# Kernel optimization log

Measured on AMD Instinct MI355X. Metric: run time of the kernel, lower is better.

The kernel has to match this reference:

```python
import jax, jax.numpy as jnp
import numpy as np

N_NODES = 100000
N_EDGES = 1000000
IN_DIM = 64
HID = 64
N_CLUSTER = 30
REG = 0.01


def glorot(key, shape):
    lim = np.sqrt(6.0 / (shape[0] + shape[1]))
    return jax.random.uniform(key, shape, jnp.float32, -lim, lim)


def setup_inputs() -> dict:
    key = jax.random.key(0)
    k1, k2, k3, k4, k5 = jax.random.split(key, 5)
    x = jax.random.normal(k1, (N_NODES, IN_DIM), jnp.float32)
    edge_index = jax.random.randint(k2, (2, N_EDGES), 0, N_NODES, jnp.int64)
    edge_attr = jax.random.uniform(k3, (N_EDGES,), jnp.float32)
    W1 = glorot(k4, (IN_DIM, HID))
    b1 = jnp.zeros((HID,), jnp.float32)
    W2 = glorot(k5, (HID, N_CLUSTER))
    b2 = jnp.zeros((N_CLUSTER,), jnp.float32)
    return {"x": x, "edge_index": edge_index, "edge_attr": edge_attr,
            "W1": W1, "b1": b1, "W2": W2, "b2": b2}


def gcn_conv(x, W, b, src, dst, w):
    # PyG GCNConv with edge weights: add self-loops (weight 1), symmetric norm.
    h = x @ W  # [N, out]
    deg = jax.ops.segment_sum(w, dst, num_segments=N_NODES) + 1.0  # self-loop
    dinv = jax.lax.rsqrt(deg)
    norm = dinv[src] * w * dinv[dst]  # [E]
    agg = jax.ops.segment_sum(norm[:, None] * h[src], dst, num_segments=N_NODES)
    agg = agg + h / deg[:, None]  # self-loop contribution: norm = 1/deg
    return agg + b


def reference(x, edge_index, edge_attr, W1, b1, W2, b2):
    src, dst = edge_index[0], edge_index[1]
    h = jax.nn.relu(gcn_conv(x, W1, b1, src, dst, edge_attr))
    # dropout p=0 -> identity
    X2 = gcn_conv(h, W2, b2, src, dst, edge_attr)
    FX = jax.nn.softmax(X2, axis=-1)  # [N, C]
    FF = jnp.sum(FX[src] * FX[dst], axis=-1)  # [E]
    NFX = jnp.log(1.0 - FX ** 2)  # [N, C]
    preg = -jnp.sum(jnp.log(1.0001 - jnp.exp(jnp.sum(NFX, axis=0))))
    loss = jnp.mean((FF - edge_attr) ** 2)
    return FX, loss + REG * preg
```

## Files before the change

kernel.cpp:

```cpp
#include <hip/hip_runtime.h>
#include <hip/hip_fp16.h>
#include <math.h>

#define N_NODES 100000
#define N_EDGES 1000000
#define IN_DIM 64
#define HID 64
#define NC 30
#define NCP 32
#define REG_C 0.01f

#define NTILES (N_NODES / 16)
#define NBUCK 391
#define EPB_A 2048
#define NBLK_A 489
#define GEMM_BLOCKS 512

typedef _Float16 half8 __attribute__((ext_vector_type(8)));
typedef _Float16 h16x4 __attribute__((ext_vector_type(4)));
typedef float f32x4 __attribute__((ext_vector_type(4)));
typedef float f32x2 __attribute__((ext_vector_type(2)));

__device__ __forceinline__ unsigned char enc_fp8(float v) {
    return (unsigned char)(__builtin_amdgcn_cvt_pk_fp8_f32(v, v, 0, false) & 0xFF);
}
__device__ __forceinline__ float dec_fp8(unsigned char b) {
    return __builtin_amdgcn_cvt_f32_fp8((int)b, 0);
}
__device__ __forceinline__ f32x4 dec_fp8x4(unsigned u) {
    f32x4 r;
    r[0] = __builtin_amdgcn_cvt_f32_fp8((int)u, 0);
    r[1] = __builtin_amdgcn_cvt_f32_fp8((int)u, 1);
    r[2] = __builtin_amdgcn_cvt_f32_fp8((int)u, 2);
    r[3] = __builtin_amdgcn_cvt_f32_fp8((int)u, 3);
    return r;
}
__device__ __forceinline__ float dot4_fp8(unsigned a, unsigned b) {
    float s = __builtin_amdgcn_cvt_f32_fp8((int)a, 0) * __builtin_amdgcn_cvt_f32_fp8((int)b, 0);
    s += __builtin_amdgcn_cvt_f32_fp8((int)a, 1) * __builtin_amdgcn_cvt_f32_fp8((int)b, 1);
    s += __builtin_amdgcn_cvt_f32_fp8((int)a, 2) * __builtin_amdgcn_cvt_f32_fp8((int)b, 2);
    s += __builtin_amdgcn_cvt_f32_fp8((int)a, 3) * __builtin_amdgcn_cvt_f32_fp8((int)b, 3);
    return s;
}

__global__ void hist_gemm(const int* __restrict__ dst, int* __restrict__ histT,
                          const float* __restrict__ X, const float* __restrict__ W,
                          unsigned char* __restrict__ H8) {
    if (blockIdx.x < NBLK_A) {
        __shared__ int cnt[NBUCK];
        for (int i = threadIdx.x; i < NBUCK; i += 256) cnt[i] = 0;
        __syncthreads();
        int e0 = blockIdx.x * EPB_A;
#pragma unroll
        for (int j = 0; j < 8; ++j) {
            int e = e0 + j * 256 + threadIdx.x;
            if (e < N_EDGES) atomicAdd(&cnt[dst[e] >> 8], 1);
        }
        __syncthreads();
        for (int b = threadIdx.x; b < NBUCK; b += 256)
            histT[b * NBLK_A + blockIdx.x] = cnt[b];
        return;
    }
    const int lane = threadIdx.x & 63;
    const int wave = threadIdx.x >> 6;
    const int qd = lane >> 4;
    const int l = lane & 15;
    half8 bfrag[2][4];
#pragma unroll
    for (int kb = 0; kb < 2; ++kb)
#pragma unroll
        for (int t = 0; t < 4; ++t)
#pragma unroll
            for (int j = 0; j < 8; ++j)
                bfrag[kb][t][j] = (_Float16)W[(kb * 32 + qd * 8 + j) * 64 + t * 16 + l];

    const int gb = blockIdx.x - NBLK_A;
    const int waveStride = GEMM_BLOCKS * 4;
    for (int ntile = gb * 4 + wave; ntile < NTILES; ntile += waveStride) {
        const int node0 = ntile * 16;
        const float* arow = X + (size_t)(node0 + l) * 64 + qd * 8;
        half8 af0, af1;
#pragma unroll
        for (int j = 0; j < 8; ++j) {
            af0[j] = (_Float16)arow[j];
            af1[j] = (_Float16)arow[32 + j];
        }
        f32x4 acc[4];
#pragma unroll
        for (int t = 0; t < 4; ++t) acc[t] = (f32x4){0.f, 0.f, 0.f, 0.f};
#pragma unroll
        for (int t = 0; t < 4; ++t) {
            acc[t] = __builtin_amdgcn_mfma_f32_16x16x32_f16(af0, bfrag[0][t], acc[t], 0, 0, 0);
            acc[t] = __builtin_amdgcn_mfma_f32_16x16x32_f16(af1, bfrag[1][t], acc[t], 0, 0, 0);
        }
#pragma unroll
        for (int t = 0; t < 4; ++t)
#pragma unroll
            for (int rr = 0; rr < 4; ++rr)
                H8[(size_t)(node0 + qd * 4 + rr) * 64 + t * 16 + l] = enc_fp8(acc[t][rr]);
    }
}

__global__ void scanA(int* __restrict__ histT, int* __restrict__ bucketTotal) {
    __shared__ int s[NBLK_A];
    int b = blockIdx.x;
    for (int i = threadIdx.x; i < NBLK_A; i += 256) s[i] = histT[b * NBLK_A + i];
    __syncthreads();
    if (threadIdx.x == 0) {
        int run = 0;
        for (int i = 0; i < NBLK_A; ++i) { int t = s[i]; s[i] = run; run += t; }
        bucketTotal[b] = run;
    }
    __syncthreads();
    for (int i = threadIdx.x; i < NBLK_A; i += 256) histT[b * NBLK_A + i] = s[i];
}

__global__ void scanB(const int* __restrict__ bucketTotal, int* __restrict__ bucketBase) {
    __shared__ int s[NBUCK];
    for (int i = threadIdx.x; i < NBUCK; i += 256) s[i] = bucketTotal[i];
    __syncthreads();
    if (threadIdx.x == 0) {
        int run = 0;
        for (int i = 0; i < NBUCK; ++i) { int t = s[i]; s[i] = run; run += t; }
    }
    __syncthreads();
    for (int i = threadIdx.x; i < NBUCK; i += 256) bucketBase[i] = s[i];
    if (threadIdx.x == 0) bucketBase[NBUCK] = N_EDGES;
}

__global__ void scatter_coarse(const int* __restrict__ src, const int* __restrict__ dst,
                               const float* __restrict__ w, const int* __restrict__ histT,
                               const int* __restrict__ bucketBase,
                               int2* __restrict__ sw, unsigned char* __restrict__ dl) {
    __shared__ int cur[NBUCK];
    int bl = blockIdx.x;
    for (int b = threadIdx.x; b < NBUCK; b += 256)
        cur[b] = bucketBase[b] + histT[b * NBLK_A + bl];
    __syncthreads();
    int e0 = bl * EPB_A;
#pragma unroll
    for (int j = 0; j < 8; ++j) {
        int e = e0 + j * 256 + threadIdx.x;
        if (e < N_EDGES) {
            int d = dst[e];
            int pos = atomicAdd(&cur[d >> 8], 1);
            sw[pos] = make_int2(src[e], __float_as_int(w[e]));
            dl[pos] = (unsigned char)(d & 255);
        }
    }
}

__global__ void bucket_deg(const int2* __restrict__ sw, const unsigned char* __restrict__ dl,
                           const int* __restrict__ bucketBase, float* __restrict__ dinv,
                           float* __restrict__ invdeg, int* __restrict__ rowptr) {
    __shared__ int cnt[256];
    __shared__ float degf[256];
    __shared__ int sc[256];
    int b = blockIdx.x, tid = threadIdx.x;
    cnt[tid] = 0; degf[tid] = 0.f;
    __syncthreads();
    int p0 = bucketBase[b], p1 = bucketBase[b + 1];
    for (int p = p0 + tid; p < p1; p += 256) {
        int d = dl[p];
        atomicAdd(&cnt[d], 1);
        atomicAdd(&degf[d], __int_as_float(sw[p].y));
    }
    __syncthreads();
    sc[tid] = cnt[tid];
    __syncthreads();
    for (int off = 1; off < 256; off <<= 1) {
        int t = (tid >= off) ? sc[tid - off] : 0;
        __syncthreads();
        sc[tid] += t;
        __syncthreads();
    }
    int node = b * 256 + tid;
    if (node < N_NODES) {
        float d = degf[tid] + 1.0f;
        dinv[node] = rsqrtf(d);
        invdeg[node] = 1.0f / d;
        rowptr[node] = p0 + sc[tid] - cnt[tid];
    }
    if (b == 0 && tid == 0) rowptr[N_NODES] = N_EDGES;
}

__global__ void bucket_scatter(const int2* __restrict__ sw, const unsigned char* __restrict__ dl,
                               const int* __restrict__ bucketBase, const int* __restrict__ rowptr,
                               const float* __restrict__ dinv,
                               int2* __restrict__ edata2, int2* __restrict__ wd) {
    __shared__ int cur[256];
    __shared__ float ldinv[256];
    int b = blockIdx.x, tid = threadIdx.x;
    int node = b * 256 + tid;
    if (node < N_NODES) { cur[tid] = rowptr[node]; ldinv[tid] = dinv[node]; }
    __syncthreads();
    int p0 = bucketBase[b], p1 = bucketBase[b + 1];
    for (int p = p0 + tid; p < p1; p += 256) {
        int d = dl[p];
        int2 r = sw[p];
        float wv = __int_as_float(r.y);
        float norm = dinv[r.x] * wv * ldinv[d];
        int pos = atomicAdd(&cur[d], 1);
        edata2[pos] = make_int2(r.x, __float_as_int(norm));
        wd[pos] = make_int2(r.y, b * 256 + d);
    }
}

__global__ void agg64_fused(const int* __restrict__ rowptr, const int2* __restrict__ edata2,
                            const unsigned char* __restrict__ H8, const float* __restrict__ invdeg,
                            const float* __restrict__ b1, _Float16* __restrict__ h2h) {
    int node = blockIdx.x * 4 + (threadIdx.x >> 6);
    if (node >= N_NODES) return;
    const int lane = threadIdx.x & 63;
    const int s = lane >> 4;
    const int q = lane & 15;
    int p = rowptr[node], end = rowptr[node + 1];
    float acc[4][4] = {};
    for (; p + 15 < end; p += 16) {
        int2 e[4];
#pragma unroll
        for (int g = 0; g < 4; ++g) e[g] = edata2[p + 4 * g + s];
        unsigned u[4];
#pragma unroll
        for (int g = 0; g < 4; ++g)
            u[g] = *(const unsigned*)(H8 + ((unsigned)e[g].x << 6) + (q << 2));
#pragma unroll
        for (int g = 0; g < 4; ++g) {
            float n = __int_as_float(e[g].y);
            f32x4 d = dec_fp8x4(u[g]);
#pragma unroll
            for (int j = 0; j < 4; ++j)
                acc[g][j] += n * d[j];
        }
    }
    {
        int r = end - p;
        int2 e[4];
#pragma unroll
        for (int g = 0; g < 4; ++g) {
            e[g] = make_int2(0, 0);
            if (4 * g + s < r) e[g] = edata2[p + 4 * g + s];
        }
        unsigned u[4];
#pragma unroll
        for (int g = 0; g < 4; ++g)
            u[g] = *(const unsigned*)(H8 + ((unsigned)e[g].x << 6) + (q << 2));
#pragma unroll
        for (int g = 0; g < 4; ++g) {
            float n = __int_as_float(e[g].y);
            f32x4 d = dec_fp8x4(u[g]);
#pragma unroll
            for (int j = 0; j < 4; ++j)
                acc[g][j] += n * d[j];
        }
    }
    float v[4];
#pragma unroll
    for (int j = 0; j < 4; ++j) {
        float t = (acc[0][j] + acc[1][j]) + (acc[2][j] + acc[3][j]);
        t += __shfl_xor(t, 16);
        t += __shfl_xor(t, 32);
        v[j] = t;
    }
    unsigned us = *(const unsigned*)(H8 + ((unsigned)node << 6) + (q << 2));
    float idg = invdeg[node];
    f32x4 bv = *(const f32x4*)(b1 + (q << 2));
    if (s == 0) {
        f32x4 ds = dec_fp8x4(us);
        h16x4 hv;
#pragma unroll
        for (int j = 0; j < 4; ++j) {
            float rj = v[j] + ds[j] * idg + bv[j];
            hv[j] = (_Float16)fmaxf(rj, 0.f);
        }
        *(h16x4*)(h2h + ((unsigned)node << 6) + (q << 2)) = hv;
    }
}

__global__ void linear30(const _Float16* __restrict__ H, const float* __restrict__ W2,
                         __half* __restrict__ HH16) {
    __shared__ float sW[64 * NC];
    __shared__ float sH[8 * 64];
    for (int i = threadIdx.x; i < 64 * NC; i += blockDim.x) sW[i] = W2[i];
    int node0 = blockIdx.x * 8;
    for (int i = threadIdx.x; i < 8 * 64; i += blockDim.x) {
        int n = node0 + (i >> 6);
        sH[i] = (n < N_NODES) ? (float)H[(size_t)n * 64 + (i & 63)] : 0.f;
    }
    __syncthreads();
    int ln = threadIdx.x >> 5;
    int c = threadIdx.x & 31;
    int node = node0 + ln;
    if (node < N_NODES) {
        float acc = 0.f;
        if (c < NC) {
#pragma unroll
            for (int k = 0; k < 64; ++k) acc += sH[ln * 64 + k] * sW[k * NC + c];
        }
        HH16[(size_t)node * NCP + c] = __float2half(acc);
    }
}

__global__ void agg30_softmax_colsum(const int* __restrict__ rowptr, const int2* __restrict__ edata2,
                                     const __half* __restrict__ HH16,
                                     const float* __restrict__ invdeg,
                                     const float* __restrict__ b2, float* __restrict__ FX,
                                     unsigned char* __restrict__ FX8,
                                     float* __restrict__ colsum_part) {
    const int lane = threadIdx.x & 63;
    const int waveInBlock = threadIdx.x >> 6;
    const int half = lane >> 5;
    const int c = lane & 31;
    const bool activeC = (c < NC);
    const int wavesTotal = gridDim.x * (blockDim.x >> 6);
    const int w0 = blockIdx.x * (blockDim.x >> 6) + waveInBlock;

    const float bb = activeC ? b2[c] : 0.f;
    float lacc = 0.f;

    for (int pair = w0; pair < N_NODES / 2; pair += wavesTotal) {
        const int node = pair * 2 + half;
        int p = rowptr[node], end = rowptr[node + 1];
        float acc[8];
#pragma unroll
        for (int k = 0; k < 8; ++k) acc[k] = 0.f;
        for (; p + 7 < end; p += 8) {
            int2 e[8];
#pragma unroll
            for (int k = 0; k < 8; ++k) e[k] = edata2[p + k];
#pragma unroll
            for (int k = 0; k < 8; ++k)
                acc[k] += __int_as_float(e[k].y) *
                          __half2float(HH16[(size_t)e[k].x * NCP + c]);
        }
        {
            int r = end - p;
            int2 e[8];
#pragma unroll
            for (int k = 0; k < 8; ++k) {
                e[k] = make_int2(0, 0);
                if (k < r) e[k] = edata2[p + k];
            }
#pragma unroll
            for (int k = 0; k < 8; ++k)
                acc[k] += __int_as_float(e[k].y) *
                          __half2float(HH16[(size_t)e[k].x * NCP + c]);
        }
        float accs = ((acc[0] + acc[1]) + (acc[2] + acc[3])) +
                     ((acc[4] + acc[5]) + (acc[6] + acc[7]));
        float selfv = __half2float(HH16[(size_t)node * NCP + c]);
        float x = activeC ? (accs + selfv * invdeg[node] + bb) : -INFINITY;
        float mx = x;
        for (int off = 16; off; off >>= 1) mx = fmaxf(mx, __shfl_xor(mx, off));
        float e = activeC ? expf(x - mx) : 0.f;
        float s = e;
        for (int off = 16; off; off >>= 1) s += __shfl_xor(s, off);
        float fx = e / s;
        if (activeC) {
            FX[(size_t)node * NC + c] = fx;
            FX8[(size_t)node * NCP + c] = enc_fp8(fx);
            lacc += log1pf(-fx * fx);
        } else {
            FX8[(size_t)node * NCP + c] = 0;
        }
    }
    lacc += __shfl_xor(lacc, 32);
    __shared__ float part[4][NC];
    if (half == 0 && activeC) part[waveInBlock][c] = lacc;
    __syncthreads();
    if (threadIdx.x < NC) {
        float v = part[0][threadIdx.x] + part[1][threadIdx.x] +
                  part[2][threadIdx.x] + part[3][threadIdx.x];
        atomicAdd(&colsum_part[(blockIdx.x & 63) * 32 + threadIdx.x], v);
    }
}

__global__ void edge_loss_sorted(const int2* __restrict__ edata2, const int2* __restrict__ wd,
                                 const unsigned char* __restrict__ FX8,
                                 float* __restrict__ mse_part) {
    int e = blockIdx.x * blockDim.x + threadIdx.x;
    float v = 0.f;
    if (e < N_EDGES) {
        int2 sn = edata2[e];
        int2 wdv = wd[e];
        const uint4* rs = (const uint4*)(FX8 + (size_t)sn.x * NCP);
        const uint4* rd = (const uint4*)(FX8 + (size_t)wdv.y * NCP);
        uint4 a0 = rs[0], a1 = rs[1];
        uint4 b0 = rd[0], b1 = rd[1];
        float ff = dot4_fp8(a0.x, b0.x) + dot4_fp8(a0.y, b0.y) +
                   dot4_fp8(a0.z, b0.z) + dot4_fp8(a0.w, b0.w) +
                   dot4_fp8(a1.x, b1.x) + dot4_fp8(a1.y, b1.y) +
                   dot4_fp8(a1.z, b1.z) + dot4_fp8(a1.w, b1.w);
        float diff = ff - __int_as_float(wdv.x);
        v = diff * diff;
    }
    for (int off = 32; off > 0; off >>= 1) v += __shfl_down(v, off);
    __shared__ float ps[4];
    int lane = threadIdx.x & 63, wv = threadIdx.x >> 6;
    if (lane == 0) ps[wv] = v;
    __syncthreads();
    if (threadIdx.x == 0)
        atomicAdd(&mse_part[blockIdx.x & 63], ps[0] + ps[1] + ps[2] + ps[3]);
}

__global__ void finalize(const float* __restrict__ colsum_part, const float* __restrict__ mse_part,
                         float* __restrict__ out_loss) {
    int t = threadIdx.x;
    float m = mse_part[t];
    for (int off = 32; off > 0; off >>= 1) m += __shfl_down(m, off);
    float term = 0.f;
    if (t < NC) {
        float s = 0.f;
        for (int k = 0; k < 64; ++k) s += colsum_part[k * 32 + t];
        term = logf(1.0001f - expf(s));
    }
    for (int off = 32; off > 0; off >>= 1) term += __shfl_down(term, off);
    if (t == 0)
        out_loss[0] = m / (float)N_EDGES - REG_C * term;
}

extern "C" void kernel_launch(void* const* d_in, const int* in_sizes, int n_in,
                              void* d_out, int out_size, void* d_ws, size_t ws_size,
                              hipStream_t stream) {
    const float* x  = (const float*)d_in[0];
    const int*   ei = (const int*)d_in[1];
    const float* ea = (const float*)d_in[2];
    const float* W1 = (const float*)d_in[3];
    const float* b1 = (const float*)d_in[4];
    const float* W2 = (const float*)d_in[5];
    const float* b2 = (const float*)d_in[6];
    const int* srcI = ei;
    const int* dstI = ei + N_EDGES;

    float* FX   = (float*)d_out;
    float* loss = FX + (size_t)N_NODES * NC;

    float* ws = (float*)d_ws;
    float*         dinv   = ws;
    float*         invdeg = ws + 100000;
    unsigned char* h8     = (unsigned char*)(ws + 200000);
    _Float16*      h2h    = (_Float16*)(ws + 1800000);
    __half*        hh16   = (__half*)(ws + 5000000);
    unsigned char* fx8    = (unsigned char*)(ws + 6600000);
    float*         colsum_part = ws + 7400000;
    float*         mse_part    = ws + 7402048;
    int*           rowptr = (int*)(ws + 7402112);
    int*           histT  = (int*)(ws + 7502114);
    int*           bucketTotal = (int*)(ws + 7693314);
    int*           bucketBase  = (int*)(ws + 7693706);
    int2*          sw     = (int2*)(ws + 7694098);
    unsigned char* dl     = (unsigned char*)(ws + 9694098);
    int2*          edata2 = (int2*)(ws + 9944098);
    int2*          wd     = (int2*)(ws + 11944098);

    hipMemsetAsync(colsum_part, 0, (2048 + 64) * sizeof(float), stream);

    hist_gemm<<<NBLK_A + GEMM_BLOCKS, 256, 0, stream>>>(dstI, histT, x, W1, h8);
    scanA<<<NBUCK, 256, 0, stream>>>(histT, bucketTotal);
    scanB<<<1, 256, 0, stream>>>(bucketTotal, bucketBase);
    scatter_coarse<<<NBLK_A, 256, 0, stream>>>(srcI, dstI, ea, histT, bucketBase, sw, dl);
    bucket_deg<<<NBUCK, 256, 0, stream>>>(sw, dl, bucketBase, dinv, invdeg, rowptr);
    bucket_scatter<<<NBUCK, 256, 0, stream>>>(sw, dl, bucketBase, rowptr, dinv, edata2, wd);
    agg64_fused<<<(N_NODES + 3) / 4, 256, 0, stream>>>(rowptr, edata2, h8, invdeg, b1, h2h);
    linear30<<<(N_NODES + 7) / 8, 256, 0, stream>>>(h2h, W2, hh16);
    agg30_softmax_colsum<<<4096, 256, 0, stream>>>(rowptr, edata2, hh16, invdeg, b2,
                                                   FX, fx8, colsum_part);
    edge_loss_sorted<<<(N_EDGES + 255) / 256, 256, 0, stream>>>(edata2, wd, fx8, mse_part);
    finalize<<<1, 64, 0, stream>>>(colsum_part, mse_part, loss);
}
```

Baseline: 295.4 us.

## Fuse W2 linear into layer-1 aggregation and drop sorted edge side array

Fuses the 64x30 linear projection into the layer-1 aggregation kernel using wave shuffles and shared W2, which removes the fp16 hidden buffer and a separate kernel launch. The second aggregation is remapped so each wave handles four nodes with two channels per lane, read as packed half2 loads. The edge loss now reads the original src/dst/weight arrays instead of a sorted wd array, so bucket_scatter no longer writes wd. The trade-off is that edge-loss gathers follow the original random edge order rather than dst-sorted order, and the fused kernel now loads all of W2 into shared memory in every block.

```diff
diff --git a/kernel.cpp b/kernel.cpp
--- a/kernel.cpp
+++ b/kernel.cpp
@@ -187,7 +187,7 @@
 __global__ void bucket_scatter(const int2* __restrict__ sw, const unsigned char* __restrict__ dl,
                                const int* __restrict__ bucketBase, const int* __restrict__ rowptr,
                                const float* __restrict__ dinv,
-                               int2* __restrict__ edata2, int2* __restrict__ wd) {
+                               int2* __restrict__ edata2) {
     __shared__ int cur[256];
     __shared__ float ldinv[256];
     int b = blockIdx.x, tid = threadIdx.x;
@@ -202,15 +202,18 @@
         float norm = dinv[r.x] * wv * ldinv[d];
         int pos = atomicAdd(&cur[d], 1);
         edata2[pos] = make_int2(r.x, __float_as_int(norm));
-        wd[pos] = make_int2(r.y, b * 256 + d);
     }
 }
 
 __global__ void agg64_fused(const int* __restrict__ rowptr, const int2* __restrict__ edata2,
                             const unsigned char* __restrict__ H8, const float* __restrict__ invdeg,
-                            const float* __restrict__ b1, _Float16* __restrict__ h2h) {
-    int node = blockIdx.x * 4 + (threadIdx.x >> 6);
-    if (node >= N_NODES) return;
+                            const float* __restrict__ b1, const float* __restrict__ W2,
+                            __half* __restrict__ HH16) {
+    __shared__ float sW[64 * NC + 2];
+    for (int i = threadIdx.x; i < 64 * NC; i += 256) sW[i] = W2[i];
+    if (threadIdx.x < 2) sW[64 * NC + threadIdx.x] = 0.f;
+
+    const int node = blockIdx.x * 4 + (threadIdx.x >> 6);
     const int lane = threadIdx.x & 63;
     const int s = lane >> 4;
     const int q = lane & 15;
@@ -265,40 +268,30 @@
     unsigned us = *(const unsigned*)(H8 + ((unsigned)node << 6) + (q << 2));
     float idg = invdeg[node];
     f32x4 bv = *(const f32x4*)(b1 + (q << 2));
-    if (s == 0) {
+    float hf[4];
+    {
         f32x4 ds = dec_fp8x4(us);
-        h16x4 hv;
 #pragma unroll
         for (int j = 0; j < 4; ++j) {
             float rj = v[j] + ds[j] * idg + bv[j];
-            hv[j] = (_Float16)fmaxf(rj, 0.f);
-        }
-        *(h16x4*)(h2h + ((unsigned)node << 6) + (q << 2)) = hv;
-    }
-}
-
-__global__ void linear30(const _Float16* __restrict__ H, const float* __restrict__ W2,
-                         __half* __restrict__ HH16) {
-    __shared__ float sW[64 * NC];
-    __shared__ float sH[8 * 64];
-    for (int i = threadIdx.x; i < 64 * NC; i += blockDim.x) sW[i] = W2[i];
-    int node0 = blockIdx.x * 8;
-    for (int i = threadIdx.x; i < 8 * 64; i += blockDim.x) {
-        int n = node0 + (i >> 6);
-        sH[i] = (n < N_NODES) ? (float)H[(size_t)n * 64 + (i & 63)] : 0.f;
-    }
-    __syncthreads();
-    int ln = threadIdx.x >> 5;
-    int c = threadIdx.x & 31;
-    int node = node0 + ln;
-    if (node < N_NODES) {
-        float acc = 0.f;
-        if (c < NC) {
-#pragma unroll
-            for (int k = 0; k < 64; ++k) acc += sH[ln * 64 + k] * sW[k * NC + c];
-        }
-        HH16[(size_t)node * NCP + c] = __float2half(acc);
-    }
+            hf[j] = (float)(_Float16)fmaxf(rj, 0.f);
+        }
+    }
+    __syncthreads();
+    const int ch = lane & 31;
+    float accw = 0.f;
+#pragma unroll
+    for (int qs = 0; qs < 8; ++qs) {
+        int q_src = ((lane >> 5) << 3) + qs;
+#pragma unroll
+        for (int j = 0; j < 4; ++j) {
+            float hk = __shfl(hf[j], q_src);
+            accw += hk * sW[(4 * q_src + j) * NC + ch];
+        }
+    }
+    accw += __shfl_xor(accw, 32);
+    if (lane < 32)
+        HH16[((size_t)node << 5) + ch] = (ch < NC) ? __float2half(accw) : __float2half(0.f);
 }
 
 __global__ void agg30_softmax_colsum(const int* __restrict__ rowptr, const int2* __restrict__ edata2,
@@ -309,64 +302,93 @@
                                      float* __restrict__ colsum_part) {
     const int lane = threadIdx.x & 63;
     const int waveInBlock = threadIdx.x >> 6;
-    const int half = lane >> 5;
-    const int c = lane & 31;
-    const bool activeC = (c < NC);
-    const int wavesTotal = gridDim.x * (blockDim.x >> 6);
-    const int w0 = blockIdx.x * (blockDim.x >> 6) + waveInBlock;
-
-    const float bb = activeC ? b2[c] : 0.f;
-    float lacc = 0.f;
-
-    for (int pair = w0; pair < N_NODES / 2; pair += wavesTotal) {
-        const int node = pair * 2 + half;
-        int p = rowptr[node], end = rowptr[node + 1];
-        float acc[8];
-#pragma unroll
-        for (int k = 0; k < 8; ++k) acc[k] = 0.f;
-        for (; p + 7 < end; p += 8) {
-            int2 e[8];
-#pragma unroll
-            for (int k = 0; k < 8; ++k) e[k] = edata2[p + k];
-#pragma unroll
-            for (int k = 0; k < 8; ++k)
-                acc[k] += __int_as_float(e[k].y) *
-                          __half2float(HH16[(size_t)e[k].x * NCP + c]);
-        }
-        {
-            int r = end - p;
-            int2 e[8];
-#pragma unroll
-            for (int k = 0; k < 8; ++k) {
-                e[k] = make_int2(0, 0);
-                if (k < r) e[k] = edata2[p + k];
-            }
-#pragma unroll
-            for (int k = 0; k < 8; ++k)
-                acc[k] += __int_as_float(e[k].y) *
-                          __half2float(HH16[(size_t)e[k].x * NCP + c]);
-        }
-        float accs = ((acc[0] + acc[1]) + (acc[2] + acc[3])) +
-                     ((acc[4] + acc[5]) + (acc[6] + acc[7]));
-        float selfv = __half2float(HH16[(size_t)node * NCP + c]);
-        float x = activeC ? (accs + selfv * invdeg[node] + bb) : -INFINITY;
-        float mx = x;
-        for (int off = 16; off; off >>= 1) mx = fmaxf(mx, __shfl_xor(mx, off));
-        float e = activeC ? expf(x - mx) : 0.f;
-        float s = e;
-        for (int off = 16; off; off >>= 1) s += __shfl_xor(s, off);
-        float fx = e / s;
-        if (activeC) {
-            FX[(size_t)node * NC + c] = fx;
-            FX8[(size_t)node * NCP + c] = enc_fp8(fx);
-            lacc += log1pf(-fx * fx);
-        } else {
-            FX8[(size_t)node * NCP + c] = 0;
-        }
-    }
-    lacc += __shfl_xor(lacc, 32);
-    __shared__ float part[4][NC];
-    if (half == 0 && activeC) part[waveInBlock][c] = lacc;
+    const int n = lane >> 4;
+    const int c2 = lane & 15;
+    const bool activeC = (c2 < 15);
+    const int node = (blockIdx.x * 4 + waveInBlock) * 4 + n;
+
+    float bb0 = activeC ? b2[2 * c2] : 0.f;
+    float bb1 = activeC ? b2[2 * c2 + 1] : 0.f;
+
+    int p = rowptr[node], end = rowptr[node + 1];
+    float a0[8], a1[8];
+#pragma unroll
+    for (int k = 0; k < 8; ++k) { a0[k] = 0.f; a1[k] = 0.f; }
+    const __half* __restrict__ Hc = HH16 + (c2 << 1);
+    for (; p + 7 < end; p += 8) {
+        int2 e[8];
+#pragma unroll
+        for (int k = 0; k < 8; ++k) e[k] = edata2[p + k];
+        unsigned h[8];
+#pragma unroll
+        for (int k = 0; k < 8; ++k)
+            h[k] = *(const unsigned*)(Hc + ((unsigned)e[k].x << 5));
+#pragma unroll
+        for (int k = 0; k < 8; ++k) {
+            float nw = __int_as_float(e[k].y);
+            float2 hf = __half22float2(*(const __half2*)&h[k]);
+            a0[k] += nw * hf.x;
+            a1[k] += nw * hf.y;
+        }
+    }
+    {
+        int r = end - p;
+        int2 e[8];
+#pragma unroll
+        for (int k = 0; k < 8; ++k) {
+            e[k] = make_int2(0, 0);
+            if (k < r) e[k] = edata2[p + k];
+        }
+        unsigned h[8];
+#pragma unroll
+        for (int k = 0; k < 8; ++k)
+            h[k] = *(const unsigned*)(Hc + ((unsigned)e[k].x << 5));
+#pragma unroll
+        for (int k = 0; k < 8; ++k) {
+            float nw = __int_as_float(e[k].y);
+            float2 hf = __half22float2(*(const __half2*)&h[k]);
+            a0[k] += nw * hf.x;
+            a1[k] += nw * hf.y;
+        }
+    }
+    float s0 = ((a0[0] + a0[1]) + (a0[2] + a0[3])) + ((a0[4] + a0[5]) + (a0[6] + a0[7]));
+    float s1 = ((a1[0] + a1[1]) + (a1[2] + a1[3])) + ((a1[4] + a1[5]) + (a1[6] + a1[7]));
+    unsigned hsu = *(const unsigned*)(Hc + ((unsigned)node << 5));
+    float2 hs = __half22float2(*(const __half2*)&hsu);
+    float idg = invdeg[node];
+    float x0 = activeC ? (s0 + hs.x * idg + bb0) : -INFINITY;
+    float x1 = activeC ? (s1 + hs.y * idg + bb1) : -INFINITY;
+    float mx = fmaxf(x0, x1);
+    mx = fmaxf(mx, __shfl_xor(mx, 1));
+    mx = fmaxf(mx, __shfl_xor(mx, 2));
+    mx = fmaxf(mx, __shfl_xor(mx, 4));
+    mx = fmaxf(mx, __shfl_xor(mx, 8));
+    float e0 = activeC ? expf(x0 - mx) : 0.f;
+    float e1 = activeC ? expf(x1 - mx) : 0.f;
+    float sum = e0 + e1;
+    sum += __shfl_xor(sum, 1);
+    sum += __shfl_xor(sum, 2);
+    sum += __shfl_xor(sum, 4);
+    sum += __shfl_xor(sum, 8);
+    float fx0 = e0 / sum;
+    float fx1 = e1 / sum;
+
+    if (activeC) {
+        *(f32x2*)(FX + (size_t)node * NC + 2 * c2) = (f32x2){fx0, fx1};
+        unsigned short pk = (unsigned short)((unsigned)enc_fp8(fx0) | ((unsigned)enc_fp8(fx1) << 8));
+        *(unsigned short*)(FX8 + ((unsigned)node << 5) + (c2 << 1)) = pk;
+    } else {
+        *(unsigned short*)(FX8 + ((unsigned)node << 5) + (c2 << 1)) = 0;
+    }
+    float lacc0 = activeC ? log1pf(-fx0 * fx0) : 0.f;
+    float lacc1 = activeC ? log1pf(-fx1 * fx1) : 0.f;
+    lacc0 += __shfl_xor(lacc0, 16); lacc0 += __shfl_xor(lacc0, 32);
+    lacc1 += __shfl_xor(lacc1, 16); lacc1 += __shfl_xor(lacc1, 32);
+    __shared__ float part[4][32];
+    if (lane < 16) {
+        part[waveInBlock][2 * c2] = lacc0;
+        part[waveInBlock][2 * c2 + 1] = lacc1;
+    }
     __syncthreads();
     if (threadIdx.x < NC) {
         float v = part[0][threadIdx.x] + part[1][threadIdx.x] +
@@ -375,23 +397,24 @@
     }
 }
 
-__global__ void edge_loss_sorted(const int2* __restrict__ edata2, const int2* __restrict__ wd,
-                                 const unsigned char* __restrict__ FX8,
-                                 float* __restrict__ mse_part) {
+__global__ void edge_loss_plain(const int* __restrict__ src, const int* __restrict__ dst,
+                                const float* __restrict__ w,
+                                const unsigned char* __restrict__ FX8,
+                                float* __restrict__ mse_part) {
     int e = blockIdx.x * blockDim.x + threadIdx.x;
     float v = 0.f;
     if (e < N_EDGES) {
-        int2 sn = edata2[e];
-        int2 wdv = wd[e];
-        const uint4* rs = (const uint4*)(FX8 + (size_t)sn.x * NCP);
-        const uint4* rd = (const uint4*)(FX8 + (size_t)wdv.y * NCP);
+        int sn = src[e];
+        int dn = dst[e];
+        const uint4* rs = (const uint4*)(FX8 + (size_t)sn * NCP);
+        const uint4* rd = (const uint4*)(FX8 + (size_t)dn * NCP);
         uint4 a0 = rs[0], a1 = rs[1];
         uint4 b0 = rd[0], b1 = rd[1];
         float ff = dot4_fp8(a0.x, b0.x) + dot4_fp8(a0.y, b0.y) +
                    dot4_fp8(a0.z, b0.z) + dot4_fp8(a0.w, b0.w) +
                    dot4_fp8(a1.x, b1.x) + dot4_fp8(a1.y, b1.y) +
                    dot4_fp8(a1.z, b1.z) + dot4_fp8(a1.w, b1.w);
-        float diff = ff - __int_as_float(wdv.x);
+        float diff = ff - w[e];
         v = diff * diff;
     }
     for (int off = 32; off > 0; off >>= 1) v += __shfl_down(v, off);
@@ -439,7 +462,6 @@
     float*         dinv   = ws;
     float*         invdeg = ws + 100000;
     unsigned char* h8     = (unsigned char*)(ws + 200000);
-    _Float16*      h2h    = (_Float16*)(ws + 1800000);
     __half*        hh16   = (__half*)(ws + 5000000);
     unsigned char* fx8    = (unsigned char*)(ws + 6600000);
     float*         colsum_part = ws + 7400000;
@@ -451,7 +473,6 @@
     int2*          sw     = (int2*)(ws + 7694098);
     unsigned char* dl     = (unsigned char*)(ws + 9694098);
     int2*          edata2 = (int2*)(ws + 9944098);
-    int2*          wd     = (int2*)(ws + 11944098);
 
     hipMemsetAsync(colsum_part, 0, (2048 + 64) * sizeof(float), stream);
 
@@ -460,11 +481,10 @@
     scanB<<<1, 256, 0, stream>>>(bucketTotal, bucketBase);
     scatter_coarse<<<NBLK_A, 256, 0, stream>>>(srcI, dstI, ea, histT, bucketBase, sw, dl);
     bucket_deg<<<NBUCK, 256, 0, stream>>>(sw, dl, bucketBase, dinv, invdeg, rowptr);
-    bucket_scatter<<<NBUCK, 256, 0, stream>>>(sw, dl, bucketBase, rowptr, dinv, edata2, wd);
-    agg64_fused<<<(N_NODES + 3) / 4, 256, 0, stream>>>(rowptr, edata2, h8, invdeg, b1, h2h);
-    linear30<<<(N_NODES + 7) / 8, 256, 0, stream>>>(h2h, W2, hh16);
-    agg30_softmax_colsum<<<4096, 256, 0, stream>>>(rowptr, edata2, hh16, invdeg, b2,
-                                                   FX, fx8, colsum_part);
-    edge_loss_sorted<<<(N_EDGES + 255) / 256, 256, 0, stream>>>(edata2, wd, fx8, mse_part);
+    bucket_scatter<<<NBUCK, 256, 0, stream>>>(sw, dl, bucketBase, rowptr, dinv, edata2);
+    agg64_fused<<<N_NODES / 4, 256, 0, stream>>>(rowptr, edata2, h8, invdeg, b1, W2, hh16);
+    agg30_softmax_colsum<<<N_NODES / 16, 256, 0, stream>>>(rowptr, edata2, hh16, invdeg, b2,
+                                                           FX, fx8, colsum_part);
+    edge_loss_plain<<<(N_EDGES + 255) / 256, 256, 0, stream>>>(srcI, dstI, ea, fx8, mse_part);
     finalize<<<1, 64, 0, stream>>>(colsum_part, mse_part, loss);
 }
```

Result: no change. 293.9 us (-0.5%).
